# Kernel tuning notes

Measured on AMD Instinct MI355X. Metric: run time of the kernel, lower is better.

The kernel has to match this reference:

```python
import jax, jax.numpy as jnp
import numpy as np


def _ln(x, g, b, eps=1e-5):
    m = x.mean(-1, keepdims=True)
    v = ((x - m) ** 2).mean(-1, keepdims=True)
    return (x - m) * jax.lax.rsqrt(v + eps) * g + b


def setup_inputs() -> dict:
    key = jax.random.key(0)
    ks = jax.random.split(key, 12)
    B, N, C, D, H, S = 32, 4096, 768, 64, 128, 7
    r = lambda k, shp: jax.random.normal(k, shp, jnp.float32) * 0.02
    return dict(
        x=jax.random.normal(ks[0], (B, N, C), jnp.float32),
        slots=jax.random.normal(ks[1], (B, S, D), jnp.float32),
        g_in=jnp.ones((C,), jnp.float32), b_in=jnp.zeros((C,), jnp.float32),
        g_sl=jnp.ones((D,), jnp.float32), b_sl=jnp.zeros((D,), jnp.float32),
        g_mlp=jnp.ones((D,), jnp.float32), b_mlp=jnp.zeros((D,), jnp.float32),
        Wq=r(ks[2], (D, D)),          # [in, out] layout; y = x @ W
        Wk=r(ks[3], (C, D)),
        Wv=r(ks[4], (C, D)),
        W_ih=r(ks[5], (D, 3 * D)),    # GRUCell input weights, gate order r,z,n
        W_hh=r(ks[6], (D, 3 * D)),
        b_ih=jnp.zeros((3 * D,), jnp.float32),
        b_hh=jnp.zeros((3 * D,), jnp.float32),
        w1=r(ks[7], (D, H)), bb1=jnp.zeros((H,), jnp.float32),
        w2=r(ks[8], (H, D)), bb2=jnp.zeros((D,), jnp.float32),
        num_iters=3,
    )


def reference(x, slots, g_in, b_in, g_sl, b_sl, g_mlp, b_mlp,
              Wq, Wk, Wv, W_ih, W_hh, b_ih, b_hh, w1, bb1, w2, bb2,
              num_iters):
    D = slots.shape[-1]
    scale = D ** -0.5
    xn = _ln(x, g_in, b_in)              # BNC
    k = xn @ Wk                          # BND
    v = xn @ Wv                          # BND
    weights = None
    for _ in range(num_iters):
        q = _ln(slots, g_sl, b_sl) @ Wq  # BSD
        logits = jnp.einsum('bsd,bnd->bsn', q, k) * scale
        # inverted attention: softmax over slots (queries)
        weights = jax.nn.softmax(logits, axis=1)               # BSN
        wn = weights / (weights.sum(-1, keepdims=True) + 1e-8)  # weighted mean over N
        attn = jnp.einsum('bsn,bnd->bsd', wn, v)               # BSD
        # GRUCell(input=attn, hidden=slots), PyTorch semantics
        gi = attn @ W_ih + b_ih
        gh = slots @ W_hh + b_hh
        ir, iz, in_ = jnp.split(gi, 3, axis=-1)
        hr, hz, hn = jnp.split(gh, 3, axis=-1)
        r = jax.nn.sigmoid(ir + hr)
        z = jax.nn.sigmoid(iz + hz)
        n = jnp.tanh(in_ + r * hn)
        slots = (1.0 - z) * n + z * slots
        # residual MLP
        slots = slots + (jax.nn.relu(_ln(slots, g_mlp, b_mlp) @ w1 + bb1) @ w2 + bb2)
    return slots, weights
```

## Files before the change

### kernel.cpp

```cpp
#include <hip/hip_runtime.h>
#include <hip/hip_bf16.h>
#include <math.h>


typedef __bf16 bf16x8 __attribute__((ext_vector_type(8)));
typedef float  f32x4  __attribute__((ext_vector_type(4)));

#define NB 32
#define NN 4096
#define NC 768
#define ND 64
#define NS 7

__device__ __forceinline__ float wave_sum64(float v) {
#pragma unroll
  for (int o = 32; o > 0; o >>= 1) v += __shfl_xor(v, o, 64);
  return v;
}

__device__ __forceinline__ void slots_ln_q(float h, int t, const float* g_sl,
                                           const float* b_sl, const float* Wq,
                                           float* y_s, float* q_out) {
  float m = wave_sum64(h) * (1.0f / 64.0f);
  float dx = h - m;
  float var = wave_sum64(dx * dx) * (1.0f / 64.0f);
  float rstd = rsqrtf(var + 1e-5f);
  y_s[t] = dx * rstd * g_sl[t] + b_sl[t];
  __syncthreads();
  float q = 0.f;
#pragma unroll 8
  for (int i = 0; i < 64; ++i) q = fmaf(y_s[i], Wq[i * 64 + t], q);
  q_out[t] = q;
}

__global__ __launch_bounds__(64) void k_prep(
    const float* __restrict__ Wk, const float* __restrict__ Wv,
    const float* __restrict__ g_in, const float* __restrict__ b_in,
    const float* __restrict__ slots_in, const float* __restrict__ g_sl,
    const float* __restrict__ b_sl, const float* __restrict__ Wq,
    __bf16* __restrict__ GWt, float* __restrict__ GWsum, float* __restrict__ BW,
    float* __restrict__ slots_ws, float* __restrict__ q_ws,
    float* __restrict__ num, float* __restrict__ den) {
  __shared__ float y_s[64];
  int t = threadIdx.x;
  int bid = blockIdx.x;
  if (bid < 128) {
    int d = bid;
    const float* W = (d < 64) ? (Wk + d) : (Wv + (d - 64));
    float sgw = 0.f, sbw = 0.f;
    for (int j = 0; j < 12; ++j) {
      int c = t + 64 * j;
      float w = W[(size_t)c * 64];
      float gw = g_in[c] * w;
      GWt[(size_t)d * NC + c] = (__bf16)gw;
      sgw += gw;
      sbw += b_in[c] * w;
    }
    sgw = wave_sum64(sgw);
    sbw = wave_sum64(sbw);
    if (t == 0) { GWsum[d] = sgw; BW[d] = sbw; }
  } else {
    int bs = bid - 128;
    float h = slots_in[bs * 64 + t];
    slots_ws[bs * 64 + t] = h;
    num[bs * 64 + t] = 0.f;
    if (t == 0) den[bs] = 0.f;
    slots_ln_q(h, t, g_sl, b_sl, Wq, y_s, q_ws + bs * 64);
  }
}

#define BM 128
#define LDA 72

__global__ __launch_bounds__(256) void k_gemm_kv(
    const float* __restrict__ x, const __bf16* __restrict__ GWt,
    const float* __restrict__ GWsum, const float* __restrict__ BW,
    float* __restrict__ kbuf, float* __restrict__ vbuf) {
  __shared__ __bf16 As[BM * LDA] __attribute__((aligned(16)));
  __shared__ __bf16 Bs[128 * LDA] __attribute__((aligned(16)));
  __shared__ float mean_s[128], rstd_s[128], gws_s[128], bw_s[128];

  int t = threadIdx.x;
  int blk = blockIdx.x;
  int lane = t & 63, wave = t >> 6;
  int wr = wave >> 1, wc = wave & 1;
  int grp = lane >> 4, lr = lane & 15;
  int r = t >> 1, half = t & 1;

  if (t < 128) { gws_s[t] = GWsum[t]; bw_s[t] = BW[t]; }

  f32x4 acc[4][4] = {};
  float s1 = 0.f, s2 = 0.f;

  const float* xrow = x + (size_t)(blk * BM + r) * NC + half * 32;
  const __bf16* grow = GWt + (size_t)r * NC + half * 32;

  for (int ck = 0; ck < 12; ++ck) {
    __syncthreads();
    {
      const float4* p4 = (const float4*)(xrow + ck * 64);
      __bf16* dst = &As[r * LDA + half * 32];
#pragma unroll
      for (int j = 0; j < 4; ++j) {
        float4 a = p4[2 * j], b = p4[2 * j + 1];
        bf16x8 pk;
        pk[0] = (__bf16)a.x; pk[1] = (__bf16)a.y; pk[2] = (__bf16)a.z; pk[3] = (__bf16)a.w;
        pk[4] = (__bf16)b.x; pk[5] = (__bf16)b.y; pk[6] = (__bf16)b.z; pk[7] = (__bf16)b.w;
        s1 += (a.x + a.y + a.z + a.w) + (b.x + b.y + b.z + b.w);
        s2 += a.x * a.x + a.y * a.y + a.z * a.z + a.w * a.w +
              b.x * b.x + b.y * b.y + b.z * b.z + b.w * b.w;
        *(bf16x8*)(dst + j * 8) = pk;
      }
    }
    {
      const uint4* p4 = (const uint4*)(grow + ck * 64);
      uint4* dst = (uint4*)&Bs[r * LDA + half * 32];
#pragma unroll
      for (int j = 0; j < 4; ++j) dst[j] = p4[j];
    }
    __syncthreads();
#pragma unroll
    for (int kk = 0; kk < 2; ++kk) {
      bf16x8 af[4], bfr[4];
#pragma unroll
      for (int i = 0; i < 4; ++i)
        af[i] = *(const bf16x8*)&As[(wr * 64 + i * 16 + lr) * LDA + kk * 32 + grp * 8];
#pragma unroll
      for (int i = 0; i < 4; ++i)
        bfr[i] = *(const bf16x8*)&Bs[(wc * 64 + i * 16 + lr) * LDA + kk * 32 + grp * 8];
#pragma unroll
      for (int i = 0; i < 4; ++i)
#pragma unroll
        for (int j = 0; j < 4; ++j)
          acc[i][j] = __builtin_amdgcn_mfma_f32_16x16x32_bf16(af[i], bfr[j], acc[i][j], 0, 0, 0);
    }
  }

  s1 += __shfl_xor(s1, 1, 64);
  s2 += __shfl_xor(s2, 1, 64);
  if (half == 0) {
    float m = s1 * (1.0f / 768.0f);
    float var = s2 * (1.0f / 768.0f) - m * m;
    mean_s[r] = m;
    rstd_s[r] = rsqrtf(var + 1e-5f);
  }
  __syncthreads();

#pragma unroll
  for (int i = 0; i < 4; ++i) {
#pragma unroll
    for (int j = 0; j < 4; ++j) {
      int colb = wc * 64 + j * 16 + lr;
      float gw = gws_s[colb], bw = bw_s[colb];
      float* obuf = (colb < 64) ? kbuf : vbuf;
      int ocol = colb & 63;
#pragma unroll
      for (int e = 0; e < 4; ++e) {
        int row = wr * 64 + i * 16 + grp * 4 + e;
        float rs = rstd_s[row], m = mean_s[row];
        float val = rs * acc[i][j][e] - m * rs * gw + bw;
        obuf[(size_t)(blk * BM + row) * 64 + ocol] = val;
      }
    }
  }
}

__global__ __launch_bounds__(256) void k_attn(
    const float* __restrict__ kbuf, const float* __restrict__ vbuf,
    const float* __restrict__ q_ws, float* __restrict__ out_w,
    float* __restrict__ num, float* __restrict__ den) {
  __shared__ float q_s[7 * 64];
  __shared__ float w_s[7 * 130];
  __shared__ float v_s[128 * 68] __attribute__((aligned(16)));
  __shared__ float den_p[28];
  __shared__ float red[7 * 4 * 64];

  int t = threadIdx.x;
  int b = blockIdx.x >> 5;
  int n0 = (blockIdx.x & 31) * 128;

  for (int idx = t; idx < 448; idx += 256) q_s[idx] = q_ws[b * 448 + idx];
  __syncthreads();

  int nl = t >> 1, dh = t & 1;
  float4 kr[8];
  const float4* kp = (const float4*)(kbuf + ((size_t)b * NN + n0 + nl) * 64 + dh * 32);
#pragma unroll
  for (int j = 0; j < 8; ++j) kr[j] = kp[j];

  float lg[7];
#pragma unroll
  for (int s = 0; s < 7; ++s) {
    const float* qv = &q_s[s * 64 + dh * 32];
    float d0 = 0.f;
#pragma unroll
    for (int j = 0; j < 8; ++j) {
      d0 = fmaf(kr[j].x, qv[4 * j + 0], d0);
      d0 = fmaf(kr[j].y, qv[4 * j + 1], d0);
      d0 = fmaf(kr[j].z, qv[4 * j + 2], d0);
      d0 = fmaf(kr[j].w, qv[4 * j + 3], d0);
    }
    d0 += __shfl_xor(d0, 1, 64);
    lg[s] = d0 * 0.125f;
  }
  float mx = lg[0];
#pragma unroll
  for (int s = 1; s < 7; ++s) mx = fmaxf(mx, lg[s]);
  float sum = 0.f;
#pragma unroll
  for (int s = 0; s < 7; ++s) { lg[s] = __expf(lg[s] - mx); sum += lg[s]; }
  float inv = 1.0f / sum;
  if (dh == 0) {
#pragma unroll
    for (int s = 0; s < 7; ++s) w_s[s * 130 + nl] = lg[s] * inv;
  }
  __syncthreads();

  for (int idx = t; idx < 896; idx += 256) {
    int s = idx >> 7, n = idx & 127;
    out_w[(size_t)b * 7 * NN + (size_t)s * NN + n0 + n] = w_s[s * 130 + n];
  }
  if (t < 28) {
    int s = t >> 2, qq = t & 3;
    float ds = 0.f;
    for (int j = 0; j < 32; ++j) ds += w_s[s * 130 + qq * 32 + j];
    den_p[t] = ds;
  }
  {
    const float4* vp = (const float4*)(vbuf + ((size_t)b * NN + n0 + nl) * 64 + dh * 32);
    float4* dst = (float4*)&v_s[nl * 68 + dh * 32];
#pragma unroll
    for (int j = 0; j < 8; ++j) dst[j] = vp[j];
  }
  __syncthreads();
  if (t < 7)
    atomicAdd(&den[b * 7 + t],
              den_p[4 * t] + den_p[4 * t + 1] + den_p[4 * t + 2] + den_p[4 * t + 3]);

  int d = t & 63, qtr = t >> 6;
  float np_[7] = {0, 0, 0, 0, 0, 0, 0};
  for (int j = 0; j < 32; ++j) {
    int n = qtr * 32 + j;
    float vv = v_s[n * 68 + d];
#pragma unroll
    for (int s = 0; s < 7; ++s) np_[s] = fmaf(w_s[s * 130 + n], vv, np_[s]);
  }
#pragma unroll
  for (int s = 0; s < 7; ++s) red[(s * 4 + qtr) * 64 + d] = np_[s];
  __syncthreads();
  for (int idx = t; idx < 448; idx += 256) {
    int s = idx >> 6, dd = idx & 63;
    float sm = red[(s * 4 + 0) * 64 + dd] + red[(s * 4 + 1) * 64 + dd] +
               red[(s * 4 + 2) * 64 + dd] + red[(s * 4 + 3) * 64 + dd];
    atomicAdd(&num[(b * 7 + s) * 64 + dd], sm);
  }
}

__global__ __launch_bounds__(64) void k_gru(
    float* __restrict__ num, float* __restrict__ den,
    float* __restrict__ slots_ws, const float* __restrict__ W_ih,
    const float* __restrict__ W_hh, const float* __restrict__ b_ih,
    const float* __restrict__ b_hh, const float* __restrict__ w1,
    const float* __restrict__ bb1, const float* __restrict__ w2,
    const float* __restrict__ bb2, const float* __restrict__ g_mlp,
    const float* __restrict__ b_mlp, const float* __restrict__ g_sl,
    const float* __restrict__ b_sl, const float* __restrict__ Wq,
    float* __restrict__ q_ws, float* __restrict__ out_slots) {
  __shared__ float att_s[64], h_s[64], y_s[64], a_s[128];
  int t = threadIdx.x;
  int bs = blockIdx.x;

  float h = slots_ws[bs * 64 + t];
  float dn = den[bs];
  float at = num[bs * 64 + t] / (dn + 1e-8f);
  att_s[t] = at;
  h_s[t] = h;
  __syncthreads();
  num[bs * 64 + t] = 0.f;
  if (t == 0) den[bs] = 0.f;

  float gi0 = b_ih[t], gi1 = b_ih[64 + t], gi2 = b_ih[128 + t];
  float gh0 = b_hh[t], gh1 = b_hh[64 + t], gh2 = b_hh[128 + t];
#pragma unroll 4
  for (int i = 0; i < 64; ++i) {
    float ai = att_s[i], hi = h_s[i];
    const float* wi = W_ih + i * 192 + t;
    const float* wh = W_hh + i * 192 + t;
    gi0 = fmaf(ai, wi[0], gi0);
    gi1 = fmaf(ai, wi[64], gi1);
    gi2 = fmaf(ai, wi[128], gi2);
    gh0 = fmaf(hi, wh[0], gh0);
    gh1 = fmaf(hi, wh[64], gh1);
    gh2 = fmaf(hi, wh[128], gh2);
  }
  float rr = 1.f / (1.f + __expf(-(gi0 + gh0)));
  float zz = 1.f / (1.f + __expf(-(gi1 + gh1)));
  float nn = tanhf(gi2 + rr * gh2);
  float hn = (1.f - zz) * nn + zz * h;

  float m = wave_sum64(hn) * (1.f / 64.f);
  float dx = hn - m;
  float var = wave_sum64(dx * dx) * (1.f / 64.f);
  float rstd = rsqrtf(var + 1e-5f);
  y_s[t] = dx * rstd * g_mlp[t] + b_mlp[t];
  __syncthreads();
  float a0 = bb1[t], a1 = bb1[64 + t];
#pragma unroll 4
  for (int i = 0; i < 64; ++i) {
    float yi = y_s[i];
    a0 = fmaf(yi, w1[i * 128 + t], a0);
    a1 = fmaf(yi, w1[i * 128 + 64 + t], a1);
  }
  a_s[t] = fmaxf(a0, 0.f);
  a_s[64 + t] = fmaxf(a1, 0.f);
  __syncthreads();
  float o = hn + bb2[t];
#pragma unroll 4
  for (int j = 0; j < 128; ++j) o = fmaf(a_s[j], w2[j * 64 + t], o);

  slots_ws[bs * 64 + t] = o;
  out_slots[bs * 64 + t] = o;
  __syncthreads();
  slots_ln_q(o, t, g_sl, b_sl, Wq, y_s, q_ws + bs * 64);
}

extern "C" void kernel_launch(void* const* d_in, const int* in_sizes, int n_in,
                              void* d_out, int out_size, void* d_ws, size_t ws_size,
                              hipStream_t stream) {
  const float* x      = (const float*)d_in[0];
  const float* slots  = (const float*)d_in[1];
  const float* g_in   = (const float*)d_in[2];
  const float* b_in   = (const float*)d_in[3];
  const float* g_sl   = (const float*)d_in[4];
  const float* b_sl   = (const float*)d_in[5];
  const float* g_mlp  = (const float*)d_in[6];
  const float* b_mlp  = (const float*)d_in[7];
  const float* Wq     = (const float*)d_in[8];
  const float* Wk     = (const float*)d_in[9];
  const float* Wv     = (const float*)d_in[10];
  const float* W_ih   = (const float*)d_in[11];
  const float* W_hh   = (const float*)d_in[12];
  const float* b_ih   = (const float*)d_in[13];
  const float* b_hh   = (const float*)d_in[14];
  const float* w1     = (const float*)d_in[15];
  const float* bb1    = (const float*)d_in[16];
  const float* w2     = (const float*)d_in[17];
  const float* bb2    = (const float*)d_in[18];

  float* out_slots = (float*)d_out;
  float* out_w     = (float*)d_out + (size_t)NB * NS * ND;

  char* ws = (char*)d_ws;
  __bf16* GWt      = (__bf16*)(ws);
  float*  GWsum    = (float*)(ws + 196608);
  float*  BW       = (float*)(ws + 197120);
  float*  q_ws     = (float*)(ws + 197632);
  float*  num      = (float*)(ws + 254976);
  float*  den      = (float*)(ws + 312320);
  float*  slots_ws = (float*)(ws + 313344);
  float*  kbuf     = (float*)(ws + 370688);
  float*  vbuf     = (float*)(ws + 370688 + 33554432);
  (void)ws_size; (void)in_sizes; (void)n_in; (void)out_size;

  k_prep<<<352, 64, 0, stream>>>(Wk, Wv, g_in, b_in, slots, g_sl, b_sl, Wq,
                                 GWt, GWsum, BW, slots_ws, q_ws, num, den);
  k_gemm_kv<<<1024, 256, 0, stream>>>(x, GWt, GWsum, BW, kbuf, vbuf);
  for (int it = 0; it < 3; ++it) {
    k_attn<<<1024, 256, 0, stream>>>(kbuf, vbuf, q_ws, out_w, num, den);
    k_gru<<<224, 64, 0, stream>>>(num, den, slots_ws, W_ih, W_hh, b_ih, b_hh,
                                  w1, bb1, w2, bb2, g_mlp, b_mlp, g_sl, b_sl,
                                  Wq, q_ws, out_slots);
  }
}
```

Before: 723.2 us.

## Store K/V in bf16, skip early weight writes, async-load B tile to LDS

The K and V intermediates are stored as bf16 instead of fp32, which halves the write traffic in the GEMM and the read traffic in each of the three attention passes. The attention-weights output is now written only on the final iteration, since earlier iterations overwrite it. The GEMM's weight tile is loaded with global_load_lds direct-to-LDS copies into an unpadded layout. The trade-offs are lower K/V precision and possible LDS bank conflicts from dropping the padding.

```diff
diff --git a/kernel.cpp b/kernel.cpp
--- a/kernel.cpp
+++ b/kernel.cpp
@@ -5,6 +5,7 @@
 
 typedef __bf16 bf16x8 __attribute__((ext_vector_type(8)));
 typedef float  f32x4  __attribute__((ext_vector_type(4)));
+typedef unsigned short u16x8 __attribute__((ext_vector_type(8)));
 
 #define NB 32
 #define NN 4096
@@ -16,6 +17,19 @@
 #pragma unroll
   for (int o = 32; o > 0; o >>= 1) v += __shfl_xor(v, o, 64);
   return v;
+}
+
+__device__ __forceinline__ float bf2f(unsigned short u) {
+  union { unsigned int i; float f; } c;
+  c.i = ((unsigned int)u) << 16;
+  return c.f;
+}
+
+__device__ __forceinline__ void glds16(const void* g, void* l) {
+  __builtin_amdgcn_global_load_lds(
+      (const __attribute__((address_space(1))) unsigned int*)(uintptr_t)g,
+      (__attribute__((address_space(3))) unsigned int*)(unsigned int)(uintptr_t)l,
+      16, 0, 0);
 }
 
 __device__ __forceinline__ void slots_ln_q(float h, int t, const float* g_sl,
@@ -75,9 +89,9 @@
 __global__ __launch_bounds__(256) void k_gemm_kv(
     const float* __restrict__ x, const __bf16* __restrict__ GWt,
     const float* __restrict__ GWsum, const float* __restrict__ BW,
-    float* __restrict__ kbuf, float* __restrict__ vbuf) {
+    __bf16* __restrict__ kbuf, __bf16* __restrict__ vbuf) {
   __shared__ __bf16 As[BM * LDA] __attribute__((aligned(16)));
-  __shared__ __bf16 Bs[128 * LDA] __attribute__((aligned(16)));
+  __shared__ __bf16 Bs[128 * 64] __attribute__((aligned(16)));
   __shared__ float mean_s[128], rstd_s[128], gws_s[128], bw_s[128];
 
   int t = threadIdx.x;
@@ -93,10 +107,15 @@
   float s1 = 0.f, s2 = 0.f;
 
   const float* xrow = x + (size_t)(blk * BM + r) * NC + half * 32;
-  const __bf16* grow = GWt + (size_t)r * NC + half * 32;
+  const char* gB = (const char*)GWt + (size_t)(wave * 32 + (lane >> 3)) * (NC * 2) +
+                   (lane & 7) * 16;
+  char* lB = (char*)&Bs[0] + wave * 4096;
 
   for (int ck = 0; ck < 12; ++ck) {
     __syncthreads();
+#pragma unroll
+    for (int j = 0; j < 4; ++j)
+      glds16(gB + ck * 128 + j * 8 * (NC * 2), lB + j * 1024);
     {
       const float4* p4 = (const float4*)(xrow + ck * 64);
       __bf16* dst = &As[r * LDA + half * 32];
@@ -112,12 +131,6 @@
         *(bf16x8*)(dst + j * 8) = pk;
       }
     }
-    {
-      const uint4* p4 = (const uint4*)(grow + ck * 64);
-      uint4* dst = (uint4*)&Bs[r * LDA + half * 32];
-#pragma unroll
-      for (int j = 0; j < 4; ++j) dst[j] = p4[j];
-    }
     __syncthreads();
 #pragma unroll
     for (int kk = 0; kk < 2; ++kk) {
@@ -127,7 +140,7 @@
         af[i] = *(const bf16x8*)&As[(wr * 64 + i * 16 + lr) * LDA + kk * 32 + grp * 8];
 #pragma unroll
       for (int i = 0; i < 4; ++i)
-        bfr[i] = *(const bf16x8*)&Bs[(wc * 64 + i * 16 + lr) * LDA + kk * 32 + grp * 8];
+        bfr[i] = *(const bf16x8*)&Bs[(wc * 64 + i * 16 + lr) * 64 + kk * 32 + grp * 8];
 #pragma unroll
       for (int i = 0; i < 4; ++i)
 #pragma unroll
@@ -152,23 +165,23 @@
     for (int j = 0; j < 4; ++j) {
       int colb = wc * 64 + j * 16 + lr;
       float gw = gws_s[colb], bw = bw_s[colb];
-      float* obuf = (colb < 64) ? kbuf : vbuf;
+      __bf16* obuf = (colb < 64) ? kbuf : vbuf;
       int ocol = colb & 63;
 #pragma unroll
       for (int e = 0; e < 4; ++e) {
         int row = wr * 64 + i * 16 + grp * 4 + e;
         float rs = rstd_s[row], m = mean_s[row];
         float val = rs * acc[i][j][e] - m * rs * gw + bw;
-        obuf[(size_t)(blk * BM + row) * 64 + ocol] = val;
+        obuf[(size_t)(blk * BM + row) * 64 + ocol] = (__bf16)val;
       }
     }
   }
 }
 
 __global__ __launch_bounds__(256) void k_attn(
-    const float* __restrict__ kbuf, const float* __restrict__ vbuf,
+    const __bf16* __restrict__ kbuf, const __bf16* __restrict__ vbuf,
     const float* __restrict__ q_ws, float* __restrict__ out_w,
-    float* __restrict__ num, float* __restrict__ den) {
+    float* __restrict__ num, float* __restrict__ den, int write_w) {
   __shared__ float q_s[7 * 64];
   __shared__ float w_s[7 * 130];
   __shared__ float v_s[128 * 68] __attribute__((aligned(16)));
@@ -183,10 +196,16 @@
   __syncthreads();
 
   int nl = t >> 1, dh = t & 1;
-  float4 kr[8];
-  const float4* kp = (const float4*)(kbuf + ((size_t)b * NN + n0 + nl) * 64 + dh * 32);
-#pragma unroll
-  for (int j = 0; j < 8; ++j) kr[j] = kp[j];
+  float kf[32];
+  {
+    const u16x8* kp = (const u16x8*)(kbuf + ((size_t)b * NN + n0 + nl) * 64 + dh * 32);
+#pragma unroll
+    for (int j = 0; j < 4; ++j) {
+      u16x8 a = kp[j];
+#pragma unroll
+      for (int m = 0; m < 8; ++m) kf[j * 8 + m] = bf2f(a[m]);
+    }
+  }
 
   float lg[7];
 #pragma unroll
@@ -194,12 +213,7 @@
     const float* qv = &q_s[s * 64 + dh * 32];
     float d0 = 0.f;
 #pragma unroll
-    for (int j = 0; j < 8; ++j) {
-      d0 = fmaf(kr[j].x, qv[4 * j + 0], d0);
-      d0 = fmaf(kr[j].y, qv[4 * j + 1], d0);
-      d0 = fmaf(kr[j].z, qv[4 * j + 2], d0);
-      d0 = fmaf(kr[j].w, qv[4 * j + 3], d0);
-    }
+    for (int j = 0; j < 32; ++j) d0 = fmaf(kf[j], qv[j], d0);
     d0 += __shfl_xor(d0, 1, 64);
     lg[s] = d0 * 0.125f;
   }
@@ -216,9 +230,11 @@
   }
   __syncthreads();
 
-  for (int idx = t; idx < 896; idx += 256) {
-    int s = idx >> 7, n = idx & 127;
-    out_w[(size_t)b * 7 * NN + (size_t)s * NN + n0 + n] = w_s[s * 130 + n];
+  if (write_w) {
+    for (int idx = t; idx < 896; idx += 256) {
+      int s = idx >> 7, n = idx & 127;
+      out_w[(size_t)b * 7 * NN + (size_t)s * NN + n0 + n] = w_s[s * 130 + n];
+    }
   }
   if (t < 28) {
     int s = t >> 2, qq = t & 3;
@@ -227,10 +243,16 @@
     den_p[t] = ds;
   }
   {
-    const float4* vp = (const float4*)(vbuf + ((size_t)b * NN + n0 + nl) * 64 + dh * 32);
+    const u16x8* vp = (const u16x8*)(vbuf + ((size_t)b * NN + n0 + nl) * 64 + dh * 32);
     float4* dst = (float4*)&v_s[nl * 68 + dh * 32];
 #pragma unroll
-    for (int j = 0; j < 8; ++j) dst[j] = vp[j];
+    for (int j = 0; j < 4; ++j) {
+      u16x8 a = vp[j];
+      float4 lo = {bf2f(a[0]), bf2f(a[1]), bf2f(a[2]), bf2f(a[3])};
+      float4 hi = {bf2f(a[4]), bf2f(a[5]), bf2f(a[6]), bf2f(a[7])};
+      dst[2 * j] = lo;
+      dst[2 * j + 1] = hi;
+    }
   }
   __syncthreads();
   if (t < 7)
@@ -358,15 +380,16 @@
   float*  num      = (float*)(ws + 254976);
   float*  den      = (float*)(ws + 312320);
   float*  slots_ws = (float*)(ws + 313344);
-  float*  kbuf     = (float*)(ws + 370688);
-  float*  vbuf     = (float*)(ws + 370688 + 33554432);
+  __bf16* kbuf     = (__bf16*)(ws + 370688);
+  __bf16* vbuf     = (__bf16*)(ws + 370688 + 16777216);
   (void)ws_size; (void)in_sizes; (void)n_in; (void)out_size;
 
   k_prep<<<352, 64, 0, stream>>>(Wk, Wv, g_in, b_in, slots, g_sl, b_sl, Wq,
                                  GWt, GWsum, BW, slots_ws, q_ws, num, den);
   k_gemm_kv<<<1024, 256, 0, stream>>>(x, GWt, GWsum, BW, kbuf, vbuf);
   for (int it = 0; it < 3; ++it) {
-    k_attn<<<1024, 256, 0, stream>>>(kbuf, vbuf, q_ws, out_w, num, den);
+    k_attn<<<1024, 256, 0, stream>>>(kbuf, vbuf, q_ws, out_w, num, den,
+                                     it == 2 ? 1 : 0);
     k_gru<<<224, 64, 0, stream>>>(num, den, slots_ws, W_ih, W_hh, b_ih, b_hh,
                                   w1, bb1, w2, bb2, g_mlp, b_mlp, g_sl, b_sl,
                                   Wq, q_ws, out_slots);
```

Result: faster. 699.0 us (-3.3%).
